# Optimization experiments

Measured on AMD Instinct MI355X. Metric: run time of the kernel, lower is better.

Reference implementation:

```python
import jax, jax.numpy as jnp
import numpy as np

VOC_SIZE = 32768
DIM = 512
NUM_TOPK = 64
BATCH = 4096


def setup_inputs() -> dict:
    key = jax.random.key(0)
    ks = jax.random.split(key, 8)
    lim = 1.0 / np.sqrt(DIM)  # kaiming_uniform(a=sqrt(5)) on [V, d] -> U(-1/sqrt(d), 1/sqrt(d))
    x = jax.random.normal(ks[0], (BATCH, DIM), dtype=jnp.float32)
    codebook = jax.random.uniform(ks[1], (VOC_SIZE, DIM), dtype=jnp.float32, minval=-lim, maxval=lim)
    Wq = jax.random.uniform(ks[2], (DIM, DIM), dtype=jnp.float32, minval=-lim, maxval=lim)
    bq = jax.random.uniform(ks[3], (DIM,), dtype=jnp.float32, minval=-lim, maxval=lim)
    Wk = jax.random.uniform(ks[4], (DIM, DIM), dtype=jnp.float32, minval=-lim, maxval=lim)
    bk = jax.random.uniform(ks[5], (DIM,), dtype=jnp.float32, minval=-lim, maxval=lim)
    Wv = jax.random.uniform(ks[6], (DIM, DIM), dtype=jnp.float32, minval=-lim, maxval=lim)
    bv = jax.random.uniform(ks[7], (DIM,), dtype=jnp.float32, minval=-lim, maxval=lim)
    return {"x": x, "codebook": codebook, "Wq": Wq, "bq": bq,
            "Wk": Wk, "bk": bk, "Wv": Wv, "bv": bv}


def reference(x, codebook, Wq, bq, Wk, bk, Wv, bv):
    # projections (torch Linear with weight stored pre-transposed as [in, out])
    q = x @ Wq + bq              # [B, d]
    k = codebook @ Wk + bk       # [V, d]
    v = codebook @ Wv + bv       # [V, d]

    dots = jnp.einsum('bd,kd->bk', q, k)              # [B, V]
    top, _ = jax.lax.top_k(dots, NUM_TOPK)            # [B, num_topk]
    thresh = top[..., -1:]                            # k-th largest value per row
    mask_value = -jnp.finfo(dots.dtype).max
    dots = jnp.where(dots < thresh, mask_value, dots)
    attn = jax.nn.softmax(dots, axis=-1)              # [B, V]
    out = jnp.einsum('bk,kd->bd', attn, v)            # [B, d]
    return out
```

## Files before the change

### kernel.cpp

```cpp
#include <hip/hip_runtime.h>
#include <cstdint>

#define VOC   32768
#define DIM   512
#define TOPK  64
#define BATCH 4096

#define KSIG     2.45f
#define EPS_SEL  0.012f
#define CAND_CAP 512
#define RES_CAP  256
#define FCAP     1024

typedef unsigned short u16;
typedef __attribute__((ext_vector_type(8))) short bf16x8;
typedef __attribute__((ext_vector_type(4))) float f32x4;

__device__ __forceinline__ u16 f2bf(float f) {
    unsigned u = __float_as_uint(f);
    unsigned r = (u + 0x7FFFu + ((u >> 16) & 1u)) >> 16;
    return (u16)r;
}
__device__ __forceinline__ float bf2f(u16 h) {
    return __uint_as_float(((unsigned)h) << 16);
// ... 76 lines not shown
            for (int i = 0; i < 4; i++)
#pragma unroll
                for (int j = 0; j < 4; j++) { acc64[i][j] += (double)acc[i][j]; acc[i][j] = 0.f; }
        }
    }

    float4 bb = make_float4(0.f, 0.f, 0.f, 0.f);
    if (bias) bb = *(const float4*)(bias + n0 + tx * 4);
#pragma unroll
    for (int i = 0; i < 4; i++) {
        float4 o;
        o.x = (F64ACC ? (float)acc64[i][0] : acc[i][0]) + bb.x;
        o.y = (F64ACC ? (float)acc64[i][1] : acc[i][1]) + bb.y;
        o.z = (F64ACC ? (float)acc64[i][2] : acc[i][2]) + bb.z;
        o.w = (F64ACC ? (float)acc64[i][3] : acc[i][3]) + bb.w;
        *(float4*)(C + (size_t)(m0 + ty * 4 + i) * N + n0 + tx * 4) = o;
    }
}

__global__ void zero_ws(unsigned* __restrict__ p, int n)
{
    int i = blockIdx.x * 256 + threadIdx.x;
    if (i < n) p[i] = 0u;
}

__device__ __forceinline__ void pack_rows_dev(int bid, int tid,
        const float* __restrict__ src, u16* __restrict__ hi,
        u16* __restrict__ lo, int R, int log2R)
{
    int idx = bid * 256 + tid;
    int c8  = idx >> log2R;
    int row = idx & (R - 1);
    const float* sp = src + (size_t)row * DIM + c8 * 8;
    float xv[8];
    *(float4*)&xv[0] = *(const float4*)sp;
    *(float4*)&xv[4] = *(const float4*)(sp + 4);
    int ks = c8 >> 2, ch = c8 & 3;
    size_t ob = ((size_t)(ks * 4 + ch) * R + row) * 8;
    u16 h[8], l[8];
#pragma unroll
    for (int j = 0; j < 8; j++) {
        h[j] = f2bf(xv[j]);
        l[j] = f2bf(xv[j] - bf2f(h[j]));
    }
    *(uint4*)(hi + ob) = *(const uint4*)h;
    if (lo) *(uint4*)(lo + ob) = *(const uint4*)l;
}

__device__ __forceinline__ void pack_bT_dev(int bid, int tid,
        const float* __restrict__ W, u16* __restrict__ hi, u16* __restrict__ lo)
{
    int idx = bid * 256 + tid;
    int n  = idx & (DIM - 1);
    int c8 = idx >> 9;
    int ks = c8 >> 2, ch = c8 & 3;
    size_t ob = ((size_t)(ks * 4 + ch) * DIM + n) * 8;
    u16 h[8], l[8];
#pragma unroll
    for (int j = 0; j < 8; j++) {
        float x = W[(size_t)(c8 * 8 + j) * DIM + n];
        h[j] = f2bf(x);
        l[j] = f2bf(x - bf2f(h[j]));
    }
    *(uint4*)(hi + ob) = *(const uint4*)h;
    *(uint4*)(lo + ob) = *(const uint4*)l;
}

__device__ __forceinline__ void cbar_dev(int bid, int tid,
        const float* __restrict__ cb, float* __restrict__ cbarsum)
{
    const int r0 = bid * 128;
    float s0 = 0.f, s1 = 0.f;
    for (int r = 0; r < 128; r++) {
        const float* rp = cb + (size_t)(r0 + r) * DIM;
        s0 += rp[tid];
        s1 += rp[tid + 256];
    }
    atomicAdd(&cbarsum[tid], s0);
    atomicAdd(&cbarsum[tid + 256], s1);
}

__device__ __forceinline__ void bias_fold_dev(int bid, int tid,
        const float* __restrict__ bq, const float* __restrict__ Wk,
        float* __restrict__ bqk)
{
    const int lane = tid & 63, wave = tid >> 6;
    const int j = bid * 4 + wave;
    const float* wr = Wk + (size_t)j * DIM + lane * 8;
    const float* bp = bq + lane * 8;
    double s = 0.0;
#pragma unroll
    for (int t = 0; t < 8; t++) s += (double)bp[t] * (double)wr[t];
#pragma unroll
    for (int off = 32; off > 0; off >>= 1) s += __shfl_down(s, off);
    if (lane == 0) bqk[j] = (float)s;
}

__device__ __forceinline__ void rowstats_dev(int bid, int tid,
        const float* __restrict__ q2, const float* __restrict__ cbarsum,
        float* __restrict__ trow, float* __restrict__ sigrow)
{
    const int lane = tid & 63, wave = tid >> 6;
    const int row = bid * 4 + wave;
    const float* qp = q2 + (size_t)row * DIM + lane * 8;
    float4 a0 = *(const float4*)qp, a1 = *(const float4*)(qp + 4);
    const float* cp = cbarsum + lane * 8;
    float4 c0 = *(const float4*)cp, c1 = *(const float4*)(cp + 4);
    float mu = a0.x*c0.x + a0.y*c0.y + a0.z*c0.z + a0.w*c0.w
             + a1.x*c1.x + a1.y*c1.y + a1.z*c1.z + a1.w*c1.w;
    float nr = a0.x*a0.x + a0.y*a0.y + a0.z*a0.z + a0.w*a0.w
             + a1.x*a1.x + a1.y*a1.y + a1.z*a1.z + a1.w*a1.w;
#pragma unroll
    for (int off = 32; off > 0; off >>= 1) {
        mu += __shfl_down(mu, off);
        nr += __shfl_down(nr, off);
    }
    if (lane == 0) {
        mu *= (1.f / VOC);
        float sig = sqrtf(nr * (1.f / 1536.f));
        trow[row] = mu + KSIG * sig;
        sigrow[row] = sig;
    }
}

__global__ __launch_bounds__(256)
void fused_prep(const float* __restrict__ x, const float* __restrict__ Wqk,
                const float* __restrict__ codebook, const float* __restrict__ Wv,
                const float* __restrict__ bq, const float* __restrict__ Wk,
                u16* __restrict__ xh, u16* __restrict__ xl,
                u16* __restrict__ wqkh, u16* __restrict__ wqkl,
                u16* __restrict__ cbh, u16* __restrict__ wvh,
                u16* __restrict__ wvl, float* __restrict__ cbarsum,
                float* __restrict__ bqk)
{
    const int b = blockIdx.x, tid = threadIdx.x;
    if (b < 1024)       pack_rows_dev(b, tid, x, xh, xl, BATCH, 12);
    else if (b < 1152)  pack_bT_dev(b - 1024, tid, Wqk, wqkh, wqkl);
    else if (b < 9344)  pack_rows_dev(b - 1152, tid, codebook, cbh, nullptr, VOC, 15);
    else if (b < 9472)  pack_bT_dev(b - 9344, tid, Wv, wvh, wvl);
    else if (b < 9728)  cbar_dev(b - 9472, tid, codebook, cbarsum);
    else                bias_fold_dev(b - 9728, tid, bq, Wk, bqk);
}

__global__ __launch_bounds__(256)
void fused_q2post(const float* __restrict__ q2, const float* __restrict__ cbarsum,
                  float* __restrict__ trow, float* __restrict__ sigrow,
                  u16* __restrict__ q2h)
{
    const int b = blockIdx.x, tid = threadIdx.x;
    if (b < 1024) rowstats_dev(b, tid, q2, cbarsum, trow, sigrow);
    else          pack_rows_dev(b - 1024, tid, q2, q2h, nullptr, BATCH, 12);
}

__global__ __launch_bounds__(256)
void pack_rows(const float* __restrict__ src, u16* __restrict__ hi,
               u16* __restrict__ lo, int R, int log2R)
{
    pack_rows_dev(blockIdx.x, threadIdx.x, src, hi, lo, R, log2R);
}

__global__ __launch_bounds__(256, 4)
void mfma_dots(const u16* __restrict__ Ah, const u16* __restrict__ Bh,
               const float* __restrict__ trow, unsigned* __restrict__ candBuf,
               unsigned* __restrict__ counters)
{
    __shared__ u16 lds[2 * 8192];

    const int tid  = threadIdx.x;
    const int lane = tid & 63;
    const int wave = tid >> 6;
    const int wm = wave >> 1, wn = wave & 1;
    const int lr = lane & 15;
    const int q  = lane >> 4;

    const int L   = blockIdx.x;
    const int xcd = L & 7;
    const int j   = L >> 3;
    const int m0  = (xcd * 4 + (j & 3)) * 128;
    const int n0  = (j >> 2) * 128;

    const int a  = wave >> 1;
    const u16* src = a ? Bh : Ah;
    const int rb   = a ? n0 : m0;
    const size_t R = a ? (size_t)VOC : (size_t)BATCH;
    const int i0   = (wave & 1) * 4;

    const size_t gstep = (size_t)4 * R * 8;
    const u16* gp0 = src + ((size_t)(((i0 + 0) >> 1)) * R + rb + ((i0 + 0) & 1) * 64 + lane) * 8;
    const u16* gp1 = src + ((size_t)(((i0 + 1) >> 1)) * R + rb + ((i0 + 1) & 1) * 64 + lane) * 8;
    const u16* gp2 = src + ((size_t)(((i0 + 2) >> 1)) * R + rb + ((i0 + 2) & 1) * 64 + lane) * 8;
    const u16* gp3 = src + ((size_t)(((i0 + 3) >> 1)) * R + rb + ((i0 + 3) & 1) * 64 + lane) * 8;
    const int loff0 = a * 4096 + (i0 + 0) * 512 + lane * 8;
    const int loff1 = a * 4096 + (i0 + 1) * 512 + lane * 8;
    const int loff2 = a * 4096 + (i0 + 2) * 512 + lane * 8;
    const int loff3 = a * 4096 + (i0 + 3) * 512 + lane * 8;

#define ISSUE(b)                                                              \
    {                                                                         \
        async16(gp0, &lds[(b) * 8192 + loff0]); gp0 += gstep;                 \
        async16(gp1, &lds[(b) * 8192 + loff1]); gp1 += gstep;                 \
        async16(gp2, &lds[(b) * 8192 + loff2]); gp2 += gstep;                 \
        async16(gp3, &lds[(b) * 8192 + loff3]); gp3 += gstep;                 \
    }

    f32x4 acc[4][4] = {};

    ISSUE(0)
    ISSUE(1)

    for (int s = 0; s < 16; s++) {
        if (s < 15) __builtin_amdgcn_s_waitcnt(0x0F74);
        else        __builtin_amdgcn_s_waitcnt(0x0F70);
        __builtin_amdgcn_s_barrier();
        const u16* base = &lds[(s & 1) * 8192];

        bf16x8 ah[4];
#pragma unroll
        for (int mt = 0; mt < 4; mt++)
            ah[mt] = *(const bf16x8*)&base[q * 1024 + (wm * 64 + mt * 16 + lr) * 8];

        __builtin_amdgcn_s_setprio(1);
#pragma unroll
        for (int nt = 0; nt < 3; nt++) {
            bf16x8 bh = *(const bf16x8*)&base[4096 + q * 1024 + (wn * 64 + nt * 16 + lr) * 8];
#pragma unroll
            for (int mt = 0; mt < 4; mt++)
                acc[mt][nt] = __builtin_amdgcn_mfma_f32_16x16x32_bf16(ah[mt], bh, acc[mt][nt], 0, 0, 0);
        }
        bf16x8 bh3 = *(const bf16x8*)&base[4096 + q * 1024 + (wn * 64 + 3 * 16 + lr) * 8];
        __builtin_amdgcn_s_setprio(0);

        __builtin_amdgcn_s_waitcnt(0xC07F);
        __builtin_amdgcn_s_barrier();
        __builtin_amdgcn_sched_barrier(0);
        if (s < 14) ISSUE(s & 1)

        __builtin_amdgcn_s_setprio(1);
#pragma unroll
        for (int mt = 0; mt < 4; mt++)
            acc[mt][3] = __builtin_amdgcn_mfma_f32_16x16x32_bf16(ah[mt], bh3, acc[mt][3], 0, 0, 0);
        __builtin_amdgcn_s_setprio(0);
    }
#undef ISSUE

#pragma unroll
    for (int mt = 0; mt < 4; mt++) {
#pragma unroll
        for (int r = 0; r < 4; r++) {
            int rowg = m0 + wm * 64 + mt * 16 + q * 4 + r;
            float tr = trow[rowg];
#pragma unroll
            for (int nt = 0; nt < 4; nt++) {
                float val = acc[mt][nt][r];
                if (val >= tr) {
                    unsigned slot = atomicAdd(&counters[rowg], 1u);
                    if (slot < CAND_CAP) {
                        unsigned s16 = enc16(f2bf(val));
                        candBuf[(size_t)rowg * CAND_CAP + slot] =
                            (s16 << 16) | (unsigned)(n0 + wn * 64 + nt * 16 + lr);
                    }
                }
            }
        }
    }
}

__global__ __launch_bounds__(256, 2)
void mfma_out(const u16* __restrict__ Ah, const u16* __restrict__ Al,
              const u16* __restrict__ Bh, const u16* __restrict__ Bl,
              const float* __restrict__ bias, float* __restrict__ Cout, int Ma)
{
    __shared__ u16 lds[2 * 16384];

    const int tid  = threadIdx.x;
    const int lane = tid & 63;
    const int wave = tid >> 6;
    const int wm = wave >> 1, wn = wave & 1;
    const int m0 = blockIdx.y * 128, n0 = blockIdx.x * 128;
    const int lr = lane & 15;
    const int q  = lane >> 4;

    f32x4 acc[4][4] = {};
    const u16* garr[4] = {Ah, Bh, Al, Bl};
    const int a = wave;
    const u16* src = garr[a];
    const bool isA = (a == 0 || a == 2);
    const int rb = isA ? m0 : n0;
    const size_t R = isA ? (size_t)Ma : (size_t)DIM;

#define VISSUE(ks, b)                                                         \
    {                                                                         \
        _Pragma("unroll")                                                     \
        for (int i_ = 0; i_ < 8; i_++) {                                      \
            const u16* gp_ = src + ((size_t)((ks) * 4 + (i_ >> 1)) * R + rb   \
                                    + (i_ & 1) * 64 + lane) * 8;              \
            async16(gp_, &lds[(b) * 16384 + a * 4096 + i_ * 512 + lane * 8]); \
        }                                                                     \
    }

    VISSUE(0, 0)

    for (int ks = 0; ks < 16; ks++) {
        __syncthreads();
        if (ks < 15) VISSUE(ks + 1, (ks + 1) & 1)
        const u16* base = &lds[(ks & 1) * 16384];

        bf16x8 ah[4], al[4];
#pragma unroll
        for (int mt = 0; mt < 4; mt++) {
            int row = wm * 64 + mt * 16 + lr;
            ah[mt] = *(const bf16x8*)&base[0 * 4096 + q * 1024 + row * 8];
            al[mt] = *(const bf16x8*)&base[2 * 4096 + q * 1024 + row * 8];
        }
#pragma unroll
        for (int nt = 0; nt < 4; nt++) {
            int col = wn * 64 + nt * 16 + lr;
            bf16x8 bh = *(const bf16x8*)&base[1 * 4096 + q * 1024 + col * 8];
            bf16x8 bl = *(const bf16x8*)&base[3 * 4096 + q * 1024 + col * 8];
#pragma unroll
            for (int mt = 0; mt < 4; mt++) {
                acc[mt][nt] = __builtin_amdgcn_mfma_f32_16x16x32_bf16(ah[mt], bh, acc[mt][nt], 0, 0, 0);
                acc[mt][nt] = __builtin_amdgcn_mfma_f32_16x16x32_bf16(ah[mt], bl, acc[mt][nt], 0, 0, 0);
                acc[mt][nt] = __builtin_amdgcn_mfma_f32_16x16x32_bf16(al[mt], bh, acc[mt][nt], 0, 0, 0);
            }
        }
    }
#undef VISSUE

#pragma unroll
    for (int mt = 0; mt < 4; mt++)
#pragma unroll
        for (int nt = 0; nt < 4; nt++) {
            int col = n0 + wn * 64 + nt * 16 + lr;
            float bb = bias[col];
#pragma unroll
            for (int r = 0; r < 4; r++) {
                int rowg = m0 + wm * 64 + mt * 16 + q * 4 + r;
                Cout[(size_t)rowg * DIM + col] = acc[mt][nt][r] + bb;
            }
        }
}

__global__ __launch_bounds__(256)
void select6(const unsigned* __restrict__ candBuf, const unsigned* __restrict__ counters,
             const float* __restrict__ trow, const float* __restrict__ q2,
             const float* __restrict__ codebook, float* __restrict__ y,
             unsigned* __restrict__ flags)
{
    __shared__ unsigned recs[CAND_CAP];
    __shared__ unsigned list[RES_CAP];
    __shared__ unsigned hist[256];
    __shared__ unsigned long long keys[RES_CAP];
    __shared__ float q2s[DIM];
    __shared__ float wArr[RES_CAP];
    __shared__ float redf[256];
    __shared__ unsigned redu[256];
    __shared__ unsigned s_R;
    __shared__ unsigned s_b1, s_rem, s_thr;

    const int tid  = threadIdx.x;
    const int lane = tid & 63;
    const int wave = tid >> 6;
    const int row  = blockIdx.x;

    const unsigned cnt = counters[row];
    if (cnt < TOPK || cnt > CAND_CAP) {
        if (tid == 0) flags[row] = 1u;
        return;
    }
    for (int i = tid; i < DIM; i += 256) q2s[i] = q2[(size_t)row * DIM + i];
    for (int i = tid; i < CAND_CAP; i += 256)
        recs[i] = (i < (int)cnt) ? candBuf[(size_t)row * CAND_CAP + i] : 0u;
    if (tid == 0) s_R = 0;
    hist[tid] = 0;
    __syncthreads();

#pragma unroll
    for (int e = 0; e < 2; e++) {
        int i = tid + e * 256;
        if (i < (int)cnt) atomicAdd(&hist[recs[i] >> 24], 1u);
    }
    __syncthreads();
    if (tid == 0) {
        unsigned c = 0; int b = 255;
        for (; b > 0; b--) {
            unsigned h = hist[b];
            if (c + h >= TOPK) break;
            c += h;
        }
        s_b1 = (unsigned)b; s_rem = TOPK - c;
    }
    __syncthreads();
    const unsigned b1 = s_b1, rem = s_rem;
    hist[tid] = 0;
    __syncthreads();

#pragma unroll
    for (int e = 0; e < 2; e++) {
        int i = tid + e * 256;
        if (i < (int)cnt && (recs[i] >> 24) == b1)
            atomicAdd(&hist[(recs[i] >> 16) & 0xFFu], 1u);
    }
    __syncthreads();
    if (tid == 0) {
        unsigned c = 0; int b = 255;
        for (; b > 0; b--) {
            unsigned h = hist[b];
            if (c + h >= rem) break;
            c += h;
        }
        s_thr = (b1 << 8) | (unsigned)b;
    }
    __syncthreads();

    const float a64  = dec16(s_thr);
    const float band = a64 - 2.f * EPS_SEL;
    if (trow[row] > band) {
        if (tid == 0) flags[row] = 1u;
        return;
    }

#pragma unroll
    for (int e = 0; e < 2; e++) {
        int i = tid + e * 256;
        if (i < (int)cnt && dec16(recs[i] >> 16) >= band) {
            unsigned p = atomicAdd(&s_R, 1u);
            if (p < RES_CAP) list[p] = recs[i];
        }
    }
    __syncthreads();
    const int R = (int)s_R;
    if (R > RES_CAP) {
        if (tid == 0) flags[row] = 1u;
        return;
    }

    for (int c = wave; c < R; c += 4) {
        unsigned idx = list[c] & 0xFFFFu;
        const float* cb = codebook + (size_t)idx * DIM + lane * 8;
        float4 c0 = *(const float4*)cb, c1 = *(const float4*)(cb + 4);
        const float* qp = &q2s[lane * 8];
        float4 a0 = *(const float4*)qp, a1 = *(const float4*)(qp + 4);
        double s = (double)a0.x * c0.x + (double)a0.y * c0.y
                 + (double)a0.z * c0.z + (double)a0.w * c0.w
                 + (double)a1.x * c1.x + (double)a1.y * c1.y
                 + (double)a1.z * c1.z + (double)a1.w * c1.w;
#pragma unroll
        for (int off = 32; off > 0; off >>= 1) s += __shfl_down(s, off);
        if (lane == 0) {
            float val = (float)s;
            unsigned b = __float_as_uint(val);
            unsigned sk = (b & 0x80000000u) ? ~b : (b | 0x80000000u);
            keys[c] = ((unsigned long long)(~sk) << 32) | idx;
        }
    }
    if (tid >= R && tid < RES_CAP) keys[tid] = ~0ULL;
    __syncthreads();

    for (int k = 2; k <= RES_CAP; k <<= 1) {
        for (int j = k >> 1; j > 0; j >>= 1) {
            int ixj = tid ^ j;
            if (ixj > tid) {
                unsigned long long a = keys[tid], b2 = keys[ixj];
                if (((tid & k) == 0) ? (a > b2) : (a < b2)) { keys[tid] = b2; keys[ixj] = a; }
            }
            __syncthreads();
        }
    }

    const unsigned threshInv = (unsigned)(keys[TOPK - 1] >> 32);
    unsigned sk0 = ~(unsigned)(keys[0] >> 32);
    const float vmax = __uint_as_float((sk0 & 0x80000000u) ? (sk0 & 0x7FFFFFFFu) : ~sk0);

    unsigned hi = (unsigned)(keys[tid] >> 32);
    bool sel = (hi <= threshInv);
    unsigned sk = ~hi;
    float val = __uint_as_float((sk & 0x80000000u) ? (sk & 0x7FFFFFFFu) : ~sk);
    float w = sel ? expf(val - vmax) : 0.f;
    wArr[tid] = w;
    redf[tid] = w;
    redu[tid] = sel ? 1u : 0u;
    __syncthreads();
    for (int s = 128; s > 0; s >>= 1) {
        if (tid < s) { redf[tid] += redf[tid + s]; redu[tid] += redu[tid + s]; }
        __syncthreads();
    }
    const float invZ = 1.0f / redf[0];
    const int selCount = (int)redu[0];

    for (int d = tid; d < DIM; d += 256) {
        float acc = 0.f;
        for (int i = 0; i < selCount; i++) {
            unsigned idx = (unsigned)(keys[i] & 0xFFFFFFFFu);
            acc += wArr[i] * codebook[(size_t)idx * DIM + d];
        }
        y[(size_t)row * DIM + d] = acc * invZ;
    }
}

__global__ __launch_bounds__(256)
void fallback_row(const unsigned* __restrict__ flags, const float* __restrict__ q2,
                  const float* __restrict__ codebook, const float* __restrict__ trow,
                  const float* __restrict__ sigrow, float* __restrict__ y)
{
    const int row = blockIdx.x;
    if (!flags[row]) return;

    __shared__ float q2s[DIM];
    __shared__ unsigned long long keys[FCAP];
    __shared__ float wArr[FCAP];
    __shared__ float redf[256];
    __shared__ unsigned redu[256];
    __shared__ unsigned s_cnt;

    const int tid = threadIdx.x;
    for (int i = tid; i < DIM; i += 256) q2s[i] = q2[(size_t)row * DIM + i];
    const float sig = sigrow[row];
    float tf = trow[row] - 0.35f * sig;
    unsigned cnt = 0;

    for (int it = 0; it < 16; it++) {
        if (tid == 0) s_cnt = 0;
        __syncthreads();
        for (int i = tid; i < VOC; i += 256) {
            const float* cb = codebook + (size_t)i * DIM;
            double s = 0.0;
            for (int d = 0; d < DIM; d += 4) {
                float4 c4 = *(const float4*)(cb + d);
                s += (double)q2s[d + 0] * (double)c4.x + (double)q2s[d + 1] * (double)c4.y
                   + (double)q2s[d + 2] * (double)c4.z + (double)q2s[d + 3] * (double)c4.w;
            }
            float vv = (float)s;
            if (vv >= tf) {
                unsigned p = atomicAdd(&s_cnt, 1u);
                if (p < FCAP) {
                    unsigned b = __float_as_uint(vv);
                    unsigned sk = (b & 0x80000000u) ? ~b : (b | 0x80000000u);
                    keys[p] = ((unsigned long long)(~sk) << 32) | (unsigned)i;
                }
            }
        }
        __syncthreads();
        cnt = s_cnt;
        if (cnt > FCAP) { tf += 0.15f * sig; continue; }
        if (cnt < TOPK) { tf -= 0.35f * sig; continue; }
        break;
    }
    if (cnt > FCAP) cnt = FCAP;
    for (int i = tid; i < FCAP; i += 256)
        if (i >= (int)cnt) keys[i] = ~0ULL;
    __syncthreads();

    for (int k = 2; k <= FCAP; k <<= 1) {
        for (int j = k >> 1; j > 0; j >>= 1) {
#pragma unroll
            for (int e = 0; e < 4; e++) {
                int i = tid + e * 256;
                int ixj = i ^ j;
                if (ixj > i) {
                    unsigned long long a = keys[i], b = keys[ixj];
                    if (((i & k) == 0) ? (a > b) : (a < b)) { keys[i] = b; keys[ixj] = a; }
                }
            }
            __syncthreads();
        }
    }

    const unsigned threshInv = (unsigned)(keys[TOPK - 1] >> 32);
    unsigned sk0 = ~(unsigned)(keys[0] >> 32);
    const float vmax = __uint_as_float((sk0 & 0x80000000u) ? (sk0 & 0x7FFFFFFFu) : ~sk0);

    float lsum = 0.f; unsigned lcnt = 0;
    for (int i = tid; i < FCAP; i += 256) {
        unsigned hi = (unsigned)(keys[i] >> 32);
        bool sel = (hi <= threshInv);
        unsigned sk = ~hi;
        float vv = __uint_as_float((sk & 0x80000000u) ? (sk & 0x7FFFFFFFu) : ~sk);
        float w = sel ? expf(vv - vmax) : 0.f;
        wArr[i] = w;
        lsum += w; lcnt += sel ? 1u : 0u;
    }
    redf[tid] = lsum; redu[tid] = lcnt;
    __syncthreads();
    for (int s = 128; s > 0; s >>= 1) {
        if (tid < s) { redf[tid] += redf[tid + s]; redu[tid] += redu[tid + s]; }
        __syncthreads();
    }
    const float invZ = 1.f / redf[0];
    const int selCount = (int)redu[0];

    for (int d = tid; d < DIM; d += 256) {
        float acc = 0.f;
        for (int i = 0; i < selCount; i++) {
            unsigned idx = (unsigned)(keys[i] & 0xFFFFFFFFu);
            acc += wArr[i] * codebook[(size_t)idx * DIM + d];
        }
        y[(size_t)row * DIM + d] = acc * invZ;
    }
}

extern "C" void kernel_launch(void* const* d_in, const int* in_sizes, int n_in,
                              void* d_out, int out_size, void* d_ws, size_t ws_size,
                              hipStream_t stream)
{
    const float* x        = (const float*)d_in[0];
    const float* codebook = (const float*)d_in[1];
    const float* Wq       = (const float*)d_in[2];
    const float* bq       = (const float*)d_in[3];
    const float* Wk       = (const float*)d_in[4];
    const float* Wv       = (const float*)d_in[6];
    const float* bv       = (const float*)d_in[7];
    float* out = (float*)d_out;

    float* q2   = (float*)d_ws;
    float* Wqk  = q2   + (size_t)BATCH * DIM;
    float* bqk  = Wqk  + (size_t)DIM * DIM;
    float* y    = bqk  + 1024;
    float* trow = y    + (size_t)BATCH * DIM;
    float* sigr = trow + BATCH;
    unsigned* counters = (unsigned*)(sigr + BATCH);
    unsigned* flags    = counters + BATCH;
    float* cbarsum     = (float*)(flags + BATCH);
    unsigned* candBuf  = (unsigned*)(cbarsum + 512);
    u16* q2h = (u16*)(candBuf + (size_t)BATCH * CAND_CAP);
    u16* cbh = q2h + (size_t)BATCH * DIM;
    u16* yh  = cbh + (size_t)VOC * DIM;
    u16* yl  = yh  + (size_t)BATCH * DIM;
    u16* wvh = yl  + (size_t)BATCH * DIM;
    u16* wvl = wvh + (size_t)DIM * DIM;

    u16* xh   = yh;
    u16* xl   = yl;
    u16* wqkh = (u16*)candBuf;
    u16* wqkl = wqkh + (size_t)DIM * DIM;

    dim3 blk(256);

    zero_ws<<<dim3(34), blk, 0, stream>>>(counters, BATCH * 2 + 512);

    gemm64<true, true><<<dim3(DIM / 64, DIM / 64), blk, 0, stream>>>(
        Wq, Wk, nullptr, Wqk, DIM, DIM, DIM);

    fused_prep<<<dim3(9856), blk, 0, stream>>>(
        x, Wqk, codebook, Wv, bq, Wk,
        xh, xl, wqkh, wqkl, cbh, wvh, wvl, cbarsum, bqk);

    mfma_out<<<dim3(DIM / 128, BATCH / 128), blk, 0, stream>>>(
        xh, xl, wqkh, wqkl, bqk, q2, BATCH);

    fused_q2post<<<dim3(2048), blk, 0, stream>>>(q2, cbarsum, trow, sigr, q2h);

    mfma_dots<<<dim3(8192), blk, 0, stream>>>(q2h, cbh, trow, candBuf, counters);

    select6<<<dim3(BATCH), blk, 0, stream>>>(
        candBuf, counters, trow, q2, codebook, y, flags);
    fallback_row<<<dim3(BATCH), blk, 0, stream>>>(
        flags, q2, codebook, trow, sigr, y);

    pack_rows<<<dim3(BATCH * 64 / 256), blk, 0, stream>>>(y, yh, yl, BATCH, 12);
    mfma_out<<<dim3(DIM / 128, BATCH / 128), blk, 0, stream>>>(
        yh, yl, wvh, wvl, bv, out, BATCH);
}
```

Baseline: 643.0 us.

## Single-buffer dots GEMM with 64-deep k-steps and narrow output GEMM tiles

Result: slower. 667.2 us (+3.8%).

```diff
diff --git a/kernel.cpp b/kernel.cpp
--- a/kernel.cpp
+++ b/kernel.cpp
@@ -264,7 +264,7 @@
                const float* __restrict__ trow, unsigned* __restrict__ candBuf,
                unsigned* __restrict__ counters)
 {
-    __shared__ u16 lds[2 * 8192];
+    __shared__ u16 lds[16384];
 
     const int tid  = threadIdx.x;
     const int lane = tid & 63;
@@ -279,67 +279,58 @@
     const int m0  = (xcd * 4 + (j & 3)) * 128;
     const int n0  = (j >> 2) * 128;
 
-    const int a  = wave >> 1;
-    const u16* src = a ? Bh : Ah;
-    const int rb   = a ? n0 : m0;
-    const size_t R = a ? (size_t)VOC : (size_t)BATCH;
-    const int i0   = (wave & 1) * 4;
-
-    const size_t gstep = (size_t)4 * R * 8;
-    const u16* gp0 = src + ((size_t)(((i0 + 0) >> 1)) * R + rb + ((i0 + 0) & 1) * 64 + lane) * 8;
-    const u16* gp1 = src + ((size_t)(((i0 + 1) >> 1)) * R + rb + ((i0 + 1) & 1) * 64 + lane) * 8;
-    const u16* gp2 = src + ((size_t)(((i0 + 2) >> 1)) * R + rb + ((i0 + 2) & 1) * 64 + lane) * 8;
-    const u16* gp3 = src + ((size_t)(((i0 + 3) >> 1)) * R + rb + ((i0 + 3) & 1) * 64 + lane) * 8;
-    const int loff0 = a * 4096 + (i0 + 0) * 512 + lane * 8;
-    const int loff1 = a * 4096 + (i0 + 1) * 512 + lane * 8;
-    const int loff2 = a * 4096 + (i0 + 2) * 512 + lane * 8;
-    const int loff3 = a * 4096 + (i0 + 3) * 512 + lane * 8;
-
-#define ISSUE(b)                                                              \
+    const size_t stepA = (size_t)8 * BATCH * 8;
+    const size_t stepB = (size_t)8 * VOC * 8;
+    const u16* gpA[4];
+    const u16* gpB[4];
+    int ldA[4], ldB[4];
+#pragma unroll
+    for (int i = 0; i < 4; i++) {
+        int u = tid + i * 256;
+        gpA[i] = Ah + ((size_t)(u >> 7) * BATCH + m0 + (u & 127)) * 8;
+        ldA[i] = u * 8;
+        gpB[i] = Bh + ((size_t)(u >> 7) * VOC + n0 + (u & 127)) * 8;
+        ldB[i] = 8192 + u * 8;
+    }
+
+#define ISSUE()                                                               \
     {                                                                         \
-        async16(gp0, &lds[(b) * 8192 + loff0]); gp0 += gstep;                 \
-        async16(gp1, &lds[(b) * 8192 + loff1]); gp1 += gstep;                 \
-        async16(gp2, &lds[(b) * 8192 + loff2]); gp2 += gstep;                 \
-        async16(gp3, &lds[(b) * 8192 + loff3]); gp3 += gstep;                 \
+        _Pragma("unroll")                                                     \
+        for (int i_ = 0; i_ < 4; i_++) { async16(gpA[i_], &lds[ldA[i_]]); gpA[i_] += stepA; } \
+        _Pragma("unroll")                                                     \
+        for (int i_ = 0; i_ < 4; i_++) { async16(gpB[i_], &lds[ldB[i_]]); gpB[i_] += stepB; } \
     }
 
     f32x4 acc[4][4] = {};
 
-    ISSUE(0)
-    ISSUE(1)
-
-    for (int s = 0; s < 16; s++) {
-        if (s < 15) __builtin_amdgcn_s_waitcnt(0x0F74);
-        else        __builtin_amdgcn_s_waitcnt(0x0F70);
+    ISSUE()
+
+    for (int s = 0; s < 8; s++) {
+        __builtin_amdgcn_s_waitcnt(0x0F70);
         __builtin_amdgcn_s_barrier();
-        const u16* base = &lds[(s & 1) * 8192];
-
-        bf16x8 ah[4];
-#pragma unroll
-        for (int mt = 0; mt < 4; mt++)
-            ah[mt] = *(const bf16x8*)&base[q * 1024 + (wm * 64 + mt * 16 + lr) * 8];
-
-        __builtin_amdgcn_s_setprio(1);
-#pragma unroll
-        for (int nt = 0; nt < 3; nt++) {
-            bf16x8 bh = *(const bf16x8*)&base[4096 + q * 1024 + (wn * 64 + nt * 16 + lr) * 8];
+
+#pragma unroll
+        for (int kk = 0; kk < 2; kk++) {
+            bf16x8 ah[4];
 #pragma unroll
             for (int mt = 0; mt < 4; mt++)
-                acc[mt][nt] = __builtin_amdgcn_mfma_f32_16x16x32_bf16(ah[mt], bh, acc[mt][nt], 0, 0, 0);
-        }
-        bf16x8 bh3 = *(const bf16x8*)&base[4096 + q * 1024 + (wn * 64 + 3 * 16 + lr) * 8];
-        __builtin_amdgcn_s_setprio(0);
-
-        __builtin_amdgcn_s_waitcnt(0xC07F);
-        __builtin_amdgcn_s_barrier();
-        __builtin_amdgcn_sched_barrier(0);
-        if (s < 14) ISSUE(s & 1)
-
-        __builtin_amdgcn_s_setprio(1);
-#pragma unroll
-        for (int mt = 0; mt < 4; mt++)
-            acc[mt][3] = __builtin_amdgcn_mfma_f32_16x16x32_bf16(ah[mt], bh3, acc[mt][3], 0, 0, 0);
-        __builtin_amdgcn_s_setprio(0);
+                ah[mt] = *(const bf16x8*)&lds[(kk * 4 + q) * 1024 + (wm * 64 + mt * 16 + lr) * 8];
+            __builtin_amdgcn_s_setprio(1);
+#pragma unroll
+            for (int nt = 0; nt < 4; nt++) {
+                bf16x8 bh = *(const bf16x8*)&lds[8192 + (kk * 4 + q) * 1024 + (wn * 64 + nt * 16 + lr) * 8];
+#pragma unroll
+                for (int mt = 0; mt < 4; mt++)
+                    acc[mt][nt] = __builtin_amdgcn_mfma_f32_16x16x32_bf16(
+                        ah[mt], bh, acc[mt][nt], 0, 0, 0);
+            }
+            __builtin_amdgcn_s_setprio(0);
+        }
+
+        if (s < 7) {
+            __syncthreads();
+            ISSUE()
+        }
     }
 #undef ISSUE
 
@@ -365,37 +356,39 @@
     }
 }
 
-__global__ __launch_bounds__(256, 2)
+__global__ __launch_bounds__(256, 3)
 void mfma_out(const u16* __restrict__ Ah, const u16* __restrict__ Al,
               const u16* __restrict__ Bh, const u16* __restrict__ Bl,
               const float* __restrict__ bias, float* __restrict__ Cout, int Ma)
 {
-    __shared__ u16 lds[2 * 16384];
+    __shared__ u16 lds[2 * 12288];
 
     const int tid  = threadIdx.x;
     const int lane = tid & 63;
     const int wave = tid >> 6;
     const int wm = wave >> 1, wn = wave & 1;
-    const int m0 = blockIdx.y * 128, n0 = blockIdx.x * 128;
+    const int m0 = blockIdx.y * 128, n0 = blockIdx.x * 64;
     const int lr = lane & 15;
     const int q  = lane >> 4;
-
-    f32x4 acc[4][4] = {};
-    const u16* garr[4] = {Ah, Bh, Al, Bl};
-    const int a = wave;
-    const u16* src = garr[a];
-    const bool isA = (a == 0 || a == 2);
-    const int rb = isA ? m0 : n0;
-    const size_t R = isA ? (size_t)Ma : (size_t)DIM;
-
-#define VISSUE(ks, b)                                                         \
-    {                                                                         \
-        _Pragma("unroll")                                                     \
-        for (int i_ = 0; i_ < 8; i_++) {                                      \
-            const u16* gp_ = src + ((size_t)((ks) * 4 + (i_ >> 1)) * R + rb   \
-                                    + (i_ & 1) * 64 + lane) * 8;              \
-            async16(gp_, &lds[(b) * 16384 + a * 4096 + i_ * 512 + lane * 8]); \
-        }                                                                     \
+    const size_t R = (size_t)Ma;
+
+    f32x4 acc[4][2] = {};
+
+#define VISSUE(ks, b)                                                          \
+    {                                                                          \
+        _Pragma("unroll")                                                      \
+        for (int i_ = 0; i_ < 2; i_++) {                                       \
+            int u_ = tid + i_ * 256;                                           \
+            size_t ai_ = ((size_t)((ks) * 4 + (u_ >> 7)) * R + m0 + (u_ & 127)) * 8; \
+            async16(Ah + ai_, &lds[(b) * 12288 + u_ * 8]);                     \
+            async16(Al + ai_, &lds[(b) * 12288 + 6144 + u_ * 8]);              \
+        }                                                                      \
+        {                                                                      \
+            int u_ = tid;                                                      \
+            size_t bi_ = ((size_t)((ks) * 4 + (u_ >> 6)) * DIM + n0 + (u_ & 63)) * 8; \
+            async16(Bh + bi_, &lds[(b) * 12288 + 4096 + u_ * 8]);              \
+            async16(Bl + bi_, &lds[(b) * 12288 + 10240 + u_ * 8]);             \
+        }                                                                      \
     }
 
     VISSUE(0, 0)
@@ -403,20 +396,20 @@
     for (int ks = 0; ks < 16; ks++) {
         __syncthreads();
         if (ks < 15) VISSUE(ks + 1, (ks + 1) & 1)
-        const u16* base = &lds[(ks & 1) * 16384];
+        const u16* base = &lds[(ks & 1) * 12288];
 
         bf16x8 ah[4], al[4];
 #pragma unroll
         for (int mt = 0; mt < 4; mt++) {
             int row = wm * 64 + mt * 16 + lr;
-            ah[mt] = *(const bf16x8*)&base[0 * 4096 + q * 1024 + row * 8];
-            al[mt] = *(const bf16x8*)&base[2 * 4096 + q * 1024 + row * 8];
-        }
-#pragma unroll
-        for (int nt = 0; nt < 4; nt++) {
-            int col = wn * 64 + nt * 16 + lr;
-            bf16x8 bh = *(const bf16x8*)&base[1 * 4096 + q * 1024 + col * 8];
-            bf16x8 bl = *(const bf16x8*)&base[3 * 4096 + q * 1024 + col * 8];
+            ah[mt] = *(const bf16x8*)&base[q * 1024 + row * 8];
+            al[mt] = *(const bf16x8*)&base[6144 + q * 1024 + row * 8];
+        }
+#pragma unroll
+        for (int nt = 0; nt < 2; nt++) {
+            int col = wn * 32 + nt * 16 + lr;
+            bf16x8 bh = *(const bf16x8*)&base[4096 + q * 512 + col * 8];
+            bf16x8 bl = *(const bf16x8*)&base[10240 + q * 512 + col * 8];
 #pragma unroll
             for (int mt = 0; mt < 4; mt++) {
                 acc[mt][nt] = __builtin_amdgcn_mfma_f32_16x16x32_bf16(ah[mt], bh, acc[mt][nt], 0, 0, 0);
@@ -430,8 +423,8 @@
 #pragma unroll
     for (int mt = 0; mt < 4; mt++)
 #pragma unroll
-        for (int nt = 0; nt < 4; nt++) {
-            int col = n0 + wn * 64 + nt * 16 + lr;
+        for (int nt = 0; nt < 2; nt++) {
+            int col = n0 + wn * 32 + nt * 16 + lr;
             float bb = bias[col];
 #pragma unroll
             for (int r = 0; r < 4; r++) {
@@ -745,7 +738,7 @@
         x, Wqk, codebook, Wv, bq, Wk,
         xh, xl, wqkh, wqkl, cbh, wvh, wvl, cbarsum, bqk);
 
-    mfma_out<<<dim3(DIM / 128, BATCH / 128), blk, 0, stream>>>(
+    mfma_out<<<dim3(DIM / 64, BATCH / 128), blk, 0, stream>>>(
         xh, xl, wqkh, wqkl, bqk, q2, BATCH);
 
     fused_q2post<<<dim3(2048), blk, 0, stream>>>(q2, cbarsum, trow, sigr, q2h);
@@ -758,6 +751,6 @@
         flags, q2, codebook, trow, sigr, y);
 
     pack_rows<<<dim3(BATCH * 64 / 256), blk, 0, stream>>>(y, yh, yl, BATCH, 12);
-    mfma_out<<<dim3(DIM / 128, BATCH / 128), blk, 0, stream>>>(
+    mfma_out<<<dim3(DIM / 64, BATCH / 128), blk, 0, stream>>>(
         yh, yl, wvh, wvl, bv, out, BATCH);
 }
```

## Fuse fallback and y packing into select kernel; narrow mfma_out tiles

Applied to the files above, without the earlier changes.

Measured after the change: 663.3 us. 1.03x slower.

```diff
diff --git a/kernel.cpp b/kernel.cpp
--- a/kernel.cpp
+++ b/kernel.cpp
@@ -252,13 +252,6 @@
     else          pack_rows_dev(b - 1024, tid, q2, q2h, nullptr, BATCH, 12);
 }
 
-__global__ __launch_bounds__(256)
-void pack_rows(const float* __restrict__ src, u16* __restrict__ hi,
-               u16* __restrict__ lo, int R, int log2R)
-{
-    pack_rows_dev(blockIdx.x, threadIdx.x, src, hi, lo, R, log2R);
-}
-
 __global__ __launch_bounds__(256, 4)
 void mfma_dots(const u16* __restrict__ Ah, const u16* __restrict__ Bh,
                const float* __restrict__ trow, unsigned* __restrict__ candBuf,
@@ -365,37 +358,39 @@
     }
 }
 
-__global__ __launch_bounds__(256, 2)
+__global__ __launch_bounds__(256, 3)
 void mfma_out(const u16* __restrict__ Ah, const u16* __restrict__ Al,
               const u16* __restrict__ Bh, const u16* __restrict__ Bl,
               const float* __restrict__ bias, float* __restrict__ Cout, int Ma)
 {
-    __shared__ u16 lds[2 * 16384];
+    __shared__ u16 lds[2 * 12288];
 
     const int tid  = threadIdx.x;
     const int lane = tid & 63;
     const int wave = tid >> 6;
     const int wm = wave >> 1, wn = wave & 1;
-    const int m0 = blockIdx.y * 128, n0 = blockIdx.x * 128;
+    const int m0 = blockIdx.y * 128, n0 = blockIdx.x * 64;
     const int lr = lane & 15;
     const int q  = lane >> 4;
-
-    f32x4 acc[4][4] = {};
-    const u16* garr[4] = {Ah, Bh, Al, Bl};
-    const int a = wave;
-    const u16* src = garr[a];
-    const bool isA = (a == 0 || a == 2);
-    const int rb = isA ? m0 : n0;
-    const size_t R = isA ? (size_t)Ma : (size_t)DIM;
-
-#define VISSUE(ks, b)                                                         \
-    {                                                                         \
-        _Pragma("unroll")                                                     \
-        for (int i_ = 0; i_ < 8; i_++) {                                      \
-            const u16* gp_ = src + ((size_t)((ks) * 4 + (i_ >> 1)) * R + rb   \
-                                    + (i_ & 1) * 64 + lane) * 8;              \
-            async16(gp_, &lds[(b) * 16384 + a * 4096 + i_ * 512 + lane * 8]); \
-        }                                                                     \
+    const size_t R = (size_t)Ma;
+
+    f32x4 acc[4][2] = {};
+
+#define VISSUE(ks, b)                                                          \
+    {                                                                          \
+        _Pragma("unroll")                                                      \
+        for (int i_ = 0; i_ < 2; i_++) {                                       \
+            int u_ = tid + i_ * 256;                                           \
+            size_t ai_ = ((size_t)((ks) * 4 + (u_ >> 7)) * R + m0 + (u_ & 127)) * 8; \
+            async16(Ah + ai_, &lds[(b) * 12288 + u_ * 8]);                     \
+            async16(Al + ai_, &lds[(b) * 12288 + 6144 + u_ * 8]);              \
+        }                                                                      \
+        {                                                                      \
+            int u_ = tid;                                                      \
+            size_t bi_ = ((size_t)((ks) * 4 + (u_ >> 6)) * DIM + n0 + (u_ & 63)) * 8; \
+            async16(Bh + bi_, &lds[(b) * 12288 + 4096 + u_ * 8]);              \
+            async16(Bl + bi_, &lds[(b) * 12288 + 10240 + u_ * 8]);             \
+        }                                                                      \
     }
 
     VISSUE(0, 0)
@@ -403,20 +398,20 @@
     for (int ks = 0; ks < 16; ks++) {
         __syncthreads();
         if (ks < 15) VISSUE(ks + 1, (ks + 1) & 1)
-        const u16* base = &lds[(ks & 1) * 16384];
+        const u16* base = &lds[(ks & 1) * 12288];
 
         bf16x8 ah[4], al[4];
 #pragma unroll
         for (int mt = 0; mt < 4; mt++) {
             int row = wm * 64 + mt * 16 + lr;
-            ah[mt] = *(const bf16x8*)&base[0 * 4096 + q * 1024 + row * 8];
-            al[mt] = *(const bf16x8*)&base[2 * 4096 + q * 1024 + row * 8];
-        }
-#pragma unroll
-        for (int nt = 0; nt < 4; nt++) {
-            int col = wn * 64 + nt * 16 + lr;
-            bf16x8 bh = *(const bf16x8*)&base[1 * 4096 + q * 1024 + col * 8];
-            bf16x8 bl = *(const bf16x8*)&base[3 * 4096 + q * 1024 + col * 8];
+            ah[mt] = *(const bf16x8*)&base[q * 1024 + row * 8];
+            al[mt] = *(const bf16x8*)&base[6144 + q * 1024 + row * 8];
+        }
+#pragma unroll
+        for (int nt = 0; nt < 2; nt++) {
+            int col = wn * 32 + nt * 16 + lr;
+            bf16x8 bh = *(const bf16x8*)&base[4096 + q * 512 + col * 8];
+            bf16x8 bl = *(const bf16x8*)&base[10240 + q * 512 + col * 8];
 #pragma unroll
             for (int mt = 0; mt < 4; mt++) {
                 acc[mt][nt] = __builtin_amdgcn_mfma_f32_16x16x32_bf16(ah[mt], bh, acc[mt][nt], 0, 0, 0);
@@ -430,8 +425,8 @@
 #pragma unroll
     for (int mt = 0; mt < 4; mt++)
 #pragma unroll
-        for (int nt = 0; nt < 4; nt++) {
-            int col = n0 + wn * 64 + nt * 16 + lr;
+        for (int nt = 0; nt < 2; nt++) {
+            int col = n0 + wn * 32 + nt * 16 + lr;
             float bb = bias[col];
 #pragma unroll
             for (int r = 0; r < 4; r++) {
@@ -442,151 +437,228 @@
 }
 
 __global__ __launch_bounds__(256)
-void select6(const unsigned* __restrict__ candBuf, const unsigned* __restrict__ counters,
-             const float* __restrict__ trow, const float* __restrict__ q2,
-             const float* __restrict__ codebook, float* __restrict__ y,
-             unsigned* __restrict__ flags)
+void select8(const unsigned* __restrict__ candBuf, const unsigned* __restrict__ counters,
+             const float* __restrict__ trow, const float* __restrict__ sigrow,
+             const float* __restrict__ q2, const float* __restrict__ codebook,
+             float* __restrict__ y, u16* __restrict__ yh, u16* __restrict__ yl)
 {
     __shared__ unsigned recs[CAND_CAP];
     __shared__ unsigned list[RES_CAP];
     __shared__ unsigned hist[256];
-    __shared__ unsigned long long keys[RES_CAP];
+    __shared__ unsigned long long keys[FCAP];
     __shared__ float q2s[DIM];
-    __shared__ float wArr[RES_CAP];
+    __shared__ float wArr[FCAP];
+    __shared__ float yrow[DIM];
     __shared__ float redf[256];
     __shared__ unsigned redu[256];
-    __shared__ unsigned s_R;
-    __shared__ unsigned s_b1, s_rem, s_thr;
+    __shared__ unsigned s_R, s_b1, s_rem, s_thr, s_cnt;
 
     const int tid  = threadIdx.x;
     const int lane = tid & 63;
     const int wave = tid >> 6;
     const int row  = blockIdx.x;
 
+    for (int i = tid; i < DIM; i += 256) q2s[i] = q2[(size_t)row * DIM + i];
+
     const unsigned cnt = counters[row];
-    if (cnt < TOPK || cnt > CAND_CAP) {
-        if (tid == 0) flags[row] = 1u;
-        return;
-    }
-    for (int i = tid; i < DIM; i += 256) q2s[i] = q2[(size_t)row * DIM + i];
-    for (int i = tid; i < CAND_CAP; i += 256)
-        recs[i] = (i < (int)cnt) ? candBuf[(size_t)row * CAND_CAP + i] : 0u;
-    if (tid == 0) s_R = 0;
-    hist[tid] = 0;
-    __syncthreads();
-
-#pragma unroll
-    for (int e = 0; e < 2; e++) {
-        int i = tid + e * 256;
-        if (i < (int)cnt) atomicAdd(&hist[recs[i] >> 24], 1u);
-    }
-    __syncthreads();
-    if (tid == 0) {
-        unsigned c = 0; int b = 255;
-        for (; b > 0; b--) {
-            unsigned h = hist[b];
-            if (c + h >= TOPK) break;
-            c += h;
-        }
-        s_b1 = (unsigned)b; s_rem = TOPK - c;
-    }
-    __syncthreads();
-    const unsigned b1 = s_b1, rem = s_rem;
-    hist[tid] = 0;
-    __syncthreads();
-
-#pragma unroll
-    for (int e = 0; e < 2; e++) {
-        int i = tid + e * 256;
-        if (i < (int)cnt && (recs[i] >> 24) == b1)
-            atomicAdd(&hist[(recs[i] >> 16) & 0xFFu], 1u);
-    }
-    __syncthreads();
-    if (tid == 0) {
-        unsigned c = 0; int b = 255;
-        for (; b > 0; b--) {
-            unsigned h = hist[b];
-            if (c + h >= rem) break;
-            c += h;
-        }
-        s_thr = (b1 << 8) | (unsigned)b;
-    }
-    __syncthreads();
-
-    const float a64  = dec16(s_thr);
-    const float band = a64 - 2.f * EPS_SEL;
-    if (trow[row] > band) {
-        if (tid == 0) flags[row] = 1u;
-        return;
-    }
-
-#pragma unroll
-    for (int e = 0; e < 2; e++) {
-        int i = tid + e * 256;
-        if (i < (int)cnt && dec16(recs[i] >> 16) >= band) {
-            unsigned p = atomicAdd(&s_R, 1u);
-            if (p < RES_CAP) list[p] = recs[i];
-        }
-    }
-    __syncthreads();
-    const int R = (int)s_R;
-    if (R > RES_CAP) {
-        if (tid == 0) flags[row] = 1u;
-        return;
-    }
-
-    for (int c = wave; c < R; c += 4) {
-        unsigned idx = list[c] & 0xFFFFu;
-        const float* cb = codebook + (size_t)idx * DIM + lane * 8;
-        float4 c0 = *(const float4*)cb, c1 = *(const float4*)(cb + 4);
-        const float* qp = &q2s[lane * 8];
-        float4 a0 = *(const float4*)qp, a1 = *(const float4*)(qp + 4);
-        double s = (double)a0.x * c0.x + (double)a0.y * c0.y
-                 + (double)a0.z * c0.z + (double)a0.w * c0.w
-                 + (double)a1.x * c1.x + (double)a1.y * c1.y
-                 + (double)a1.z * c1.z + (double)a1.w * c1.w;
-#pragma unroll
-        for (int off = 32; off > 0; off >>= 1) s += __shfl_down(s, off);
-        if (lane == 0) {
-            float val = (float)s;
-            unsigned b = __float_as_uint(val);
-            unsigned sk = (b & 0x80000000u) ? ~b : (b | 0x80000000u);
-            keys[c] = ((unsigned long long)(~sk) << 32) | idx;
-        }
-    }
-    if (tid >= R && tid < RES_CAP) keys[tid] = ~0ULL;
-    __syncthreads();
-
-    for (int k = 2; k <= RES_CAP; k <<= 1) {
-        for (int j = k >> 1; j > 0; j >>= 1) {
-            int ixj = tid ^ j;
-            if (ixj > tid) {
-                unsigned long long a = keys[tid], b2 = keys[ixj];
-                if (((tid & k) == 0) ? (a > b2) : (a < b2)) { keys[tid] = b2; keys[ixj] = a; }
+    bool fb = (cnt < TOPK || cnt > CAND_CAP);
+    int selCount = 0;
+    float invZ = 1.f;
+
+    if (!fb) {
+        for (int i = tid; i < CAND_CAP; i += 256)
+            recs[i] = (i < (int)cnt) ? candBuf[(size_t)row * CAND_CAP + i] : 0u;
+        if (tid == 0) s_R = 0;
+        hist[tid] = 0;
+        __syncthreads();
+
+#pragma unroll
+        for (int e = 0; e < 2; e++) {
+            int i = tid + e * 256;
+            if (i < (int)cnt) atomicAdd(&hist[recs[i] >> 24], 1u);
+        }
+        __syncthreads();
+        if (tid == 0) {
+            unsigned c = 0; int b = 255;
+            for (; b > 0; b--) {
+                unsigned h = hist[b];
+                if (c + h >= TOPK) break;
+                c += h;
+            }
+            s_b1 = (unsigned)b; s_rem = TOPK - c;
+        }
+        __syncthreads();
+        const unsigned b1 = s_b1, rem = s_rem;
+        hist[tid] = 0;
+        __syncthreads();
+
+#pragma unroll
+        for (int e = 0; e < 2; e++) {
+            int i = tid + e * 256;
+            if (i < (int)cnt && (recs[i] >> 24) == b1)
+                atomicAdd(&hist[(recs[i] >> 16) & 0xFFu], 1u);
+        }
+        __syncthreads();
+        if (tid == 0) {
+            unsigned c = 0; int b = 255;
+            for (; b > 0; b--) {
+                unsigned h = hist[b];
+                if (c + h >= rem) break;
+                c += h;
+            }
+            s_thr = (b1 << 8) | (unsigned)b;
+        }
+        __syncthreads();
+
+        const float a64  = dec16(s_thr);
+        const float band = a64 - 2.f * EPS_SEL;
+        if (trow[row] > band) fb = true;
+
+        if (!fb) {
+#pragma unroll
+            for (int e = 0; e < 2; e++) {
+                int i = tid + e * 256;
+                if (i < (int)cnt && dec16(recs[i] >> 16) >= band) {
+                    unsigned p = atomicAdd(&s_R, 1u);
+                    if (p < RES_CAP) list[p] = recs[i];
+                }
             }
             __syncthreads();
-        }
-    }
-
-    const unsigned threshInv = (unsigned)(keys[TOPK - 1] >> 32);
-    unsigned sk0 = ~(unsigned)(keys[0] >> 32);
-    const float vmax = __uint_as_float((sk0 & 0x80000000u) ? (sk0 & 0x7FFFFFFFu) : ~sk0);
-
-    unsigned hi = (unsigned)(keys[tid] >> 32);
-    bool sel = (hi <= threshInv);
-    unsigned sk = ~hi;
-    float val = __uint_as_float((sk & 0x80000000u) ? (sk & 0x7FFFFFFFu) : ~sk);
-    float w = sel ? expf(val - vmax) : 0.f;
-    wArr[tid] = w;
-    redf[tid] = w;
-    redu[tid] = sel ? 1u : 0u;
-    __syncthreads();
-    for (int s = 128; s > 0; s >>= 1) {
-        if (tid < s) { redf[tid] += redf[tid + s]; redu[tid] += redu[tid + s]; }
-        __syncthreads();
-    }
-    const float invZ = 1.0f / redf[0];
-    const int selCount = (int)redu[0];
+            const int R = (int)s_R;
+            if (R > RES_CAP) fb = true;
+
+            if (!fb) {
+                for (int c = wave; c < R; c += 4) {
+                    unsigned idx = list[c] & 0xFFFFu;
+                    const float* cb = codebook + (size_t)idx * DIM + lane * 8;
+                    float4 c0 = *(const float4*)cb, c1 = *(const float4*)(cb + 4);
+                    const float* qp = &q2s[lane * 8];
+                    float4 a0 = *(const float4*)qp, a1 = *(const float4*)(qp + 4);
+                    double s = (double)a0.x * c0.x + (double)a0.y * c0.y
+                             + (double)a0.z * c0.z + (double)a0.w * c0.w
+                             + (double)a1.x * c1.x + (double)a1.y * c1.y
+                             + (double)a1.z * c1.z + (double)a1.w * c1.w;
+#pragma unroll
+                    for (int off = 32; off > 0; off >>= 1) s += __shfl_down(s, off);
+                    if (lane == 0) {
+                        float val = (float)s;
+                        unsigned b = __float_as_uint(val);
+                        unsigned sk = (b & 0x80000000u) ? ~b : (b | 0x80000000u);
+                        keys[c] = ((unsigned long long)(~sk) << 32) | idx;
+                    }
+                }
+                if (tid >= R && tid < RES_CAP) keys[tid] = ~0ULL;
+                __syncthreads();
+
+                for (int k = 2; k <= RES_CAP; k <<= 1) {
+                    for (int j = k >> 1; j > 0; j >>= 1) {
+                        int ixj = tid ^ j;
+                        if (ixj > tid) {
+                            unsigned long long a = keys[tid], b2 = keys[ixj];
+                            if (((tid & k) == 0) ? (a > b2) : (a < b2)) { keys[tid] = b2; keys[ixj] = a; }
+                        }
+                        __syncthreads();
+                    }
+                }
+
+                const unsigned threshInv = (unsigned)(keys[TOPK - 1] >> 32);
+                unsigned sk0 = ~(unsigned)(keys[0] >> 32);
+                const float vmax = __uint_as_float((sk0 & 0x80000000u) ? (sk0 & 0x7FFFFFFFu) : ~sk0);
+
+                unsigned hi = (unsigned)(keys[tid] >> 32);
+                bool sel = (hi <= threshInv);
+                unsigned sk = ~hi;
+                float val = __uint_as_float((sk & 0x80000000u) ? (sk & 0x7FFFFFFFu) : ~sk);
+                float w = sel ? expf(val - vmax) : 0.f;
+                wArr[tid] = w;
+                redf[tid] = w;
+                redu[tid] = sel ? 1u : 0u;
+                __syncthreads();
+                for (int s = 128; s > 0; s >>= 1) {
+                    if (tid < s) { redf[tid] += redf[tid + s]; redu[tid] += redu[tid + s]; }
+                    __syncthreads();
+                }
+                invZ = 1.0f / redf[0];
+                selCount = (int)redu[0];
+            }
+        }
+    }
+
+    if (fb) {
+        const float sig = sigrow[row];
+        float tf = trow[row] - 0.35f * sig;
+        unsigned fcnt = 0;
+
+        for (int it = 0; it < 16; it++) {
+            if (tid == 0) s_cnt = 0;
+            __syncthreads();
+            for (int i = tid; i < VOC; i += 256) {
+                const float* cb = codebook + (size_t)i * DIM;
+                double s = 0.0;
+                for (int d = 0; d < DIM; d += 4) {
+                    float4 c4 = *(const float4*)(cb + d);
+                    s += (double)q2s[d + 0] * (double)c4.x + (double)q2s[d + 1] * (double)c4.y
+                       + (double)q2s[d + 2] * (double)c4.z + (double)q2s[d + 3] * (double)c4.w;
+                }
+                float vv = (float)s;
+                if (vv >= tf) {
+                    unsigned p = atomicAdd(&s_cnt, 1u);
+                    if (p < FCAP) {
+                        unsigned b = __float_as_uint(vv);
+                        unsigned sk = (b & 0x80000000u) ? ~b : (b | 0x80000000u);
+                        keys[p] = ((unsigned long long)(~sk) << 32) | (unsigned)i;
+                    }
+                }
+            }
+            __syncthreads();
+            fcnt = s_cnt;
+            if (fcnt > FCAP) { tf += 0.15f * sig; continue; }
+            if (fcnt < TOPK) { tf -= 0.35f * sig; continue; }
+            break;
+        }
+        if (fcnt > FCAP) fcnt = FCAP;
+        for (int i = tid; i < FCAP; i += 256)
+            if (i >= (int)fcnt) keys[i] = ~0ULL;
+        __syncthreads();
+
+        for (int k = 2; k <= FCAP; k <<= 1) {
+            for (int j = k >> 1; j > 0; j >>= 1) {
+#pragma unroll
+                for (int e = 0; e < 4; e++) {
+                    int i = tid + e * 256;
+                    int ixj = i ^ j;
+                    if (ixj > i) {
+                        unsigned long long a = keys[i], b = keys[ixj];
+                        if (((i & k) == 0) ? (a > b) : (a < b)) { keys[i] = b; keys[ixj] = a; }
+                    }
+                }
+                __syncthreads();
+            }
+        }
+
+        const unsigned threshInv = (unsigned)(keys[TOPK - 1] >> 32);
+        unsigned sk0 = ~(unsigned)(keys[0] >> 32);
+        const float vmax = __uint_as_float((sk0 & 0x80000000u) ? (sk0 & 0x7FFFFFFFu) : ~sk0);
+
+        float lsum = 0.f; unsigned lcnt = 0;
+        for (int i = tid; i < FCAP; i += 256) {
+            unsigned hi = (unsigned)(keys[i] >> 32);
+            bool sel = (hi <= threshInv);
+            unsigned sk = ~hi;
+            float vv = __uint_as_float((sk & 0x80000000u) ? (sk & 0x7FFFFFFFu) : ~sk);
+            float w = sel ? expf(vv - vmax) : 0.f;
+            wArr[i] = w;
+            lsum += w; lcnt += sel ? 1u : 0u;
+        }
+        redf[tid] = lsum; redu[tid] = lcnt;
+        __syncthreads();
+        for (int s = 128; s > 0; s >>= 1) {
+            if (tid < s) { redf[tid] += redf[tid + s]; redu[tid] += redu[tid + s]; }
+            __syncthreads();
+        }
+        invZ = 1.f / redf[0];
+        selCount = (int)redu[0];
+    }
 
     for (int d = tid; d < DIM; d += 256) {
         float acc = 0.f;
@@ -594,108 +666,23 @@
             unsigned idx = (unsigned)(keys[i] & 0xFFFFFFFFu);
             acc += wArr[i] * codebook[(size_t)idx * DIM + d];
         }
-        y[(size_t)row * DIM + d] = acc * invZ;
-    }
-}
-
-__global__ __launch_bounds__(256)
-void fallback_row(const unsigned* __restrict__ flags, const float* __restrict__ q2,
-                  const float* __restrict__ codebook, const float* __restrict__ trow,
-                  const float* __restrict__ sigrow, float* __restrict__ y)
-{
-    const int row = blockIdx.x;
-    if (!flags[row]) return;
-
-    __shared__ float q2s[DIM];
-    __shared__ unsigned long long keys[FCAP];
-    __shared__ float wArr[FCAP];
-    __shared__ float redf[256];
-    __shared__ unsigned redu[256];
-    __shared__ unsigned s_cnt;
-
-    const int tid = threadIdx.x;
-    for (int i = tid; i < DIM; i += 256) q2s[i] = q2[(size_t)row * DIM + i];
-    const float sig = sigrow[row];
-    float tf = trow[row] - 0.35f * sig;
-    unsigned cnt = 0;
-
-    for (int it = 0; it < 16; it++) {
-        if (tid == 0) s_cnt = 0;
-        __syncthreads();
-        for (int i = tid; i < VOC; i += 256) {
-            const float* cb = codebook + (size_t)i * DIM;
-            double s = 0.0;
-            for (int d = 0; d < DIM; d += 4) {
-                float4 c4 = *(const float4*)(cb + d);
-                s += (double)q2s[d + 0] * (double)c4.x + (double)q2s[d + 1] * (double)c4.y
-                   + (double)q2s[d + 2] * (double)c4.z + (double)q2s[d + 3] * (double)c4.w;
-            }
-            float vv = (float)s;
-            if (vv >= tf) {
-                unsigned p = atomicAdd(&s_cnt, 1u);
-                if (p < FCAP) {
-                    unsigned b = __float_as_uint(vv);
-                    unsigned sk = (b & 0x80000000u) ? ~b : (b | 0x80000000u);
-                    keys[p] = ((unsigned long long)(~sk) << 32) | (unsigned)i;
-                }
-            }
-        }
-        __syncthreads();
-        cnt = s_cnt;
-        if (cnt > FCAP) { tf += 0.15f * sig; continue; }
-        if (cnt < TOPK) { tf -= 0.35f * sig; continue; }
-        break;
-    }
-    if (cnt > FCAP) cnt = FCAP;
-    for (int i = tid; i < FCAP; i += 256)
-        if (i >= (int)cnt) keys[i] = ~0ULL;
+        float v = acc * invZ;
+        y[(size_t)row * DIM + d] = v;
+        yrow[d] = v;
+    }
     __syncthreads();
-
-    for (int k = 2; k <= FCAP; k <<= 1) {
-        for (int j = k >> 1; j > 0; j >>= 1) {
-#pragma unroll
-            for (int e = 0; e < 4; e++) {
-                int i = tid + e * 256;
-                int ixj = i ^ j;
-                if (ixj > i) {
-                    unsigned long long a = keys[i], b = keys[ixj];
-                    if (((i & k) == 0) ? (a > b) : (a < b)) { keys[i] = b; keys[ixj] = a; }
-                }
-            }
-            __syncthreads();
-        }
-    }
-
-    const unsigned threshInv = (unsigned)(keys[TOPK - 1] >> 32);
-    unsigned sk0 = ~(unsigned)(keys[0] >> 32);
-    const float vmax = __uint_as_float((sk0 & 0x80000000u) ? (sk0 & 0x7FFFFFFFu) : ~sk0);
-
-    float lsum = 0.f; unsigned lcnt = 0;
-    for (int i = tid; i < FCAP; i += 256) {
-        unsigned hi = (unsigned)(keys[i] >> 32);
-        bool sel = (hi <= threshInv);
-        unsigned sk = ~hi;
-        float vv = __uint_as_float((sk & 0x80000000u) ? (sk & 0x7FFFFFFFu) : ~sk);
-        float w = sel ? expf(vv - vmax) : 0.f;
-        wArr[i] = w;
-        lsum += w; lcnt += sel ? 1u : 0u;
-    }
-    redf[tid] = lsum; redu[tid] = lcnt;
-    __syncthreads();
-    for (int s = 128; s > 0; s >>= 1) {
-        if (tid < s) { redf[tid] += redf[tid + s]; redu[tid] += redu[tid + s]; }
-        __syncthreads();
-    }
-    const float invZ = 1.f / redf[0];
-    const int selCount = (int)redu[0];
-
-    for (int d = tid; d < DIM; d += 256) {
-        float acc = 0.f;
-        for (int i = 0; i < selCount; i++) {
-            unsigned idx = (unsigned)(keys[i] & 0xFFFFFFFFu);
-            acc += wArr[i] * codebook[(size_t)idx * DIM + d];
-        }
-        y[(size_t)row * DIM + d] = acc * invZ;
+    if (tid < 64) {
+        const int c8 = tid;
+        u16 h[8], l[8];
+#pragma unroll
+        for (int j = 0; j < 8; j++) {
+            float xv = yrow[c8 * 8 + j];
+            h[j] = f2bf(xv);
+            l[j] = f2bf(xv - bf2f(h[j]));
+        }
+        size_t ob = ((size_t)c8 * BATCH + row) * 8;
+        *(uint4*)(yh + ob) = *(const uint4*)h;
+        *(uint4*)(yl + ob) = *(const uint4*)l;
     }
 }
 
@@ -745,19 +732,16 @@
         x, Wqk, codebook, Wv, bq, Wk,
         xh, xl, wqkh, wqkl, cbh, wvh, wvl, cbarsum, bqk);
 
-    mfma_out<<<dim3(DIM / 128, BATCH / 128), blk, 0, stream>>>(
+    mfma_out<<<dim3(DIM / 64, BATCH / 128), blk, 0, stream>>>(
         xh, xl, wqkh, wqkl, bqk, q2, BATCH);
 
     fused_q2post<<<dim3(2048), blk, 0, stream>>>(q2, cbarsum, trow, sigr, q2h);
 
     mfma_dots<<<dim3(8192), blk, 0, stream>>>(q2h, cbh, trow, candBuf, counters);
 
-    select6<<<dim3(BATCH), blk, 0, stream>>>(
-        candBuf, counters, trow, q2, codebook, y, flags);
-    fallback_row<<<dim3(BATCH), blk, 0, stream>>>(
-        flags, q2, codebook, trow, sigr, y);
-
-    pack_rows<<<dim3(BATCH * 64 / 256), blk, 0, stream>>>(y, yh, yl, BATCH, 12);
-    mfma_out<<<dim3(DIM / 128, BATCH / 128), blk, 0, stream>>>(
+    select8<<<dim3(BATCH), blk, 0, stream>>>(
+        candBuf, counters, trow, sigr, q2, codebook, y, yh, yl);
+
+    mfma_out<<<dim3(DIM / 64, BATCH / 128), blk, 0, stream>>>(
         yh, yl, wvh, wvl, bv, out, BATCH);
 }
```
